# Performance work log

Hardware: AMD Instinct MI355X
Metric: run time of the kernel (lower is better)

## Reference

```python
import jax, jax.numpy as jnp
import numpy as np

K, R, D = 200000, 64, 1024
N_IDS = 16384
BITS = 4
GROUP = 32


def group_quantize(w, bits, group_size):
    """Group-wise symmetric fake-quant along the last dim (STE in bwd)."""
    last = w.shape[-1]
    g = min(group_size, last)
    n_groups = last // g
    wg = w.reshape(w.shape[:-1] + (n_groups, g))
    amax = jnp.clip(jnp.max(jnp.abs(wg), axis=-1, keepdims=True), 1e-8, None)
    q_max = (1 << (bits - 1)) - 1  # matches torch `1 << bits - 1` precedence
    scale = amax / q_max
    q = jnp.clip(jnp.round(wg / scale), -q_max, q_max) * scale
    # straight-through estimator: forward = q, backward = identity w.r.t. wg
    wq = wg + jax.lax.stop_gradient(q - wg)
    return wq.reshape(w.shape)


def setup_inputs() -> dict:
    key = jax.random.key(0)
    k1, k2, k3 = jax.random.split(key, 3)
    U = jax.random.normal(k1, (K, R), dtype=jnp.float32)
    B = jax.random.normal(k2, (R, D), dtype=jnp.float32)
    local_ids = jax.random.randint(k3, (N_IDS,), 0, K, dtype=jnp.int64 if jax.config.read('jax_enable_x64') else jnp.int32)
    return {"U": U, "B": B, "local_ids": local_ids}


def reference(U, B, local_ids):
    # row(): quantize ALL of U, gather selected rows, matmul with quantized B
    Uq = group_quantize(U, BITS, min(GROUP, R))   # [K, r]
    Bq = group_quantize(B, BITS, min(GROUP, D))   # [r, d]
    return Uq[local_ids] @ Bq                      # [N, d]
```

## Files before the change

### kernel.cpp

```cpp
#include <hip/hip_runtime.h>


#define R_DIM 64
#define D_DIM 1024
#define N_IDS 16384

#define BM 64
#define BN 128
#define LDS_STRIDE 72
#define OT_STRIDE 132

#define NB_QB 256
#define NB_QU 4096

typedef __attribute__((ext_vector_type(8))) __bf16 bf16x8;
typedef __attribute__((ext_vector_type(4))) float f32x4;

__device__ inline unsigned short f32_to_bf16_rne(float f) {
  union { float f; unsigned int u; } c; c.f = f;
  unsigned int u = c.u;
  u += 0x7fffu + ((u >> 16) & 1u);
  return (unsigned short)(u >> 16);
}

__device__ inline float bf16_bits_to_f32(unsigned short h) {
  union { unsigned int u; float f; } c; c.u = ((unsigned int)h) << 16;
  return c.f;
}

__device__ inline void quant_split(float w, float a, unsigned short* hi, unsigned short* lo) {
  double amax  = fmax((double)a, 1e-8);
  double scale = amax / 7.0;
  double t     = (double)w / scale;
  double q     = fmin(fmax(rint(t), -7.0), 7.0) * scale;
  float qf = (float)q;
  unsigned short h = f32_to_bf16_rne(qf);
  *hi = h;
  *lo = f32_to_bf16_rne(qf - bf16_bits_to_f32(h));
}

__device__ inline float group_amax32(float w) {
  float a = fabsf(w);
  a = fmaxf(a, __shfl_xor(a, 1));
  a = fmaxf(a, __shfl_xor(a, 2));
  a = fmaxf(a, __shfl_xor(a, 4));
  a = fmaxf(a, __shfl_xor(a, 8));
  a = fmaxf(a, __shfl_xor(a, 16));
  return a;
}

__global__ __launch_bounds__(256) void quant_fused_kernel(
    const float* __restrict__ U, const float* __restrict__ B,
    const int* __restrict__ ids,
    unsigned short* __restrict__ BqT_hi, unsigned short* __restrict__ BqT_lo,
    unsigned short* __restrict__ Uq_hi,  unsigned short* __restrict__ Uq_lo) {
  const int bid = blockIdx.x;
  if (bid < NB_QB) {
    int e = bid * 256 + threadIdx.x;
    int r = e >> 10;
    int c = e & 1023;
    float w = B[e];
    unsigned short hi, lo;
    quant_split(w, group_amax32(w), &hi, &lo);
    BqT_hi[c * R_DIM + r] = hi;
    BqT_lo[c * R_DIM + r] = lo;
  } else {
    int e = (bid - NB_QB) * 256 + threadIdx.x;
    int n = e >> 6;
    int r = e & 63;
    float w = __builtin_nontemporal_load(&U[(size_t)ids[n] * R_DIM + r]);
    unsigned short hi, lo;
    quant_split(w, group_amax32(w), &hi, &lo);
    Uq_hi[e] = hi;
    Uq_lo[e] = lo;
  }
}

__global__ __launch_bounds__(256) void gemm_kernel(
    const unsigned short* __restrict__ Uq_hi, const unsigned short* __restrict__ Uq_lo,
    const unsigned short* __restrict__ BqT_hi, const unsigned short* __restrict__ BqT_lo,
    float* __restrict__ out) {
  __shared__ char smem[2 * BN * LDS_STRIDE * 2];
  unsigned short* bt_hi = (unsigned short*)smem;
  unsigned short* bt_lo = bt_hi + BN * LDS_STRIDE;
  float* ot = (float*)smem;

  const int tid  = threadIdx.x;
  const int lane = tid & 63;
  const int wave = tid >> 6;
  const int bx   = blockIdx.x;
  const int nb   = bx & 7;
  const int mb   = bx >> 3;
  const int n0   = nb * BN;

  {
    const uint4* src_hi = (const uint4*)(BqT_hi + (size_t)n0 * R_DIM);
    const uint4* src_lo = (const uint4*)(BqT_lo + (size_t)n0 * R_DIM);
    #pragma unroll
    for (int it = 0; it < 4; ++it) {
      int c = tid + it * 256;
      int row = c >> 3, off = c & 7;
      *(uint4*)&bt_hi[row * LDS_STRIDE + off * 8] = src_hi[c];
      *(uint4*)&bt_lo[row * LDS_STRIDE + off * 8] = src_lo[c];
    }
  }

  const int m0    = mb * BM + wave * 16;
  const int arow  = m0 + (lane & 15);
  const int koff  = (lane >> 4) * 8;
  const int nlane = lane & 15;

  bf16x8 afrag_hi[2], afrag_lo[2];
  #pragma unroll
  for (int s = 0; s < 2; ++s) {
    afrag_hi[s] = *(const bf16x8*)&Uq_hi[(size_t)arow * R_DIM + s * 32 + koff];
    afrag_lo[s] = *(const bf16x8*)&Uq_lo[(size_t)arow * R_DIM + s * 32 + koff];
  }

  __syncthreads();

  f32x4 acc[8];
  #pragma unroll
  for (int nf = 0; nf < 8; ++nf) acc[nf] = (f32x4){0.f, 0.f, 0.f, 0.f};

  #pragma unroll
  for (int nf = 0; nf < 8; ++nf) {
    #pragma unroll
    for (int s = 0; s < 2; ++s) {
      const int boff = (nf * 16 + nlane) * LDS_STRIDE + s * 32 + koff;
      union { uint4 u; bf16x8 b; } bh, bl;
      bh.u = *(const uint4*)&bt_hi[boff];
      bl.u = *(const uint4*)&bt_lo[boff];
      acc[nf] = __builtin_amdgcn_mfma_f32_16x16x32_bf16(afrag_hi[s], bh.b, acc[nf], 0, 0, 0);
      acc[nf] = __builtin_amdgcn_mfma_f32_16x16x32_bf16(afrag_hi[s], bl.b, acc[nf], 0, 0, 0);
      acc[nf] = __builtin_amdgcn_mfma_f32_16x16x32_bf16(afrag_lo[s], bh.b, acc[nf], 0, 0, 0);
    }
  }

  __syncthreads();

  float* w = ot + wave * 16 * OT_STRIDE;
  {
    const int r0 = (lane >> 4) << 2;
    #pragma unroll
    for (int nf = 0; nf < 8; ++nf) {
      #pragma unroll
      for (int i = 0; i < 4; ++i) {
        w[(r0 + i) * OT_STRIDE + nlane + nf * 16] = acc[nf][i];
      }
    }
  }
  #pragma unroll
  for (int j = 0; j < 8; ++j) {
    const int row = j * 2 + (lane >> 5);
    f32x4 v = *(const f32x4*)&w[row * OT_STRIDE + (lane & 31) * 4];
    __builtin_nontemporal_store(v,
        (f32x4*)&out[(size_t)(m0 + row) * D_DIM + n0 + (lane & 31) * 4]);
  }
}

extern "C" void kernel_launch(void* const* d_in, const int* in_sizes, int n_in,
                              void* d_out, int out_size, void* d_ws, size_t ws_size,
                              hipStream_t stream) {
  const float* U   = (const float*)d_in[0];
  const float* B   = (const float*)d_in[1];
  const int*   ids = (const int*)d_in[2];
  float* out = (float*)d_out;

  unsigned short* BqT_hi = (unsigned short*)d_ws;
  unsigned short* BqT_lo = BqT_hi + R_DIM * D_DIM;
  unsigned short* Uq_hi  = BqT_lo + R_DIM * D_DIM;
  unsigned short* Uq_lo  = Uq_hi + (size_t)N_IDS * R_DIM;

  quant_fused_kernel<<<NB_QB + NB_QU, 256, 0, stream>>>(U, B, ids, BqT_hi, BqT_lo, Uq_hi, Uq_lo);
  gemm_kernel<<<(N_IDS / BM) * (D_DIM / BN), 256, 0, stream>>>(Uq_hi, Uq_lo, BqT_hi, BqT_lo, out);
}
```

Measured before the change: 30.68 us.

## Fuse U gather and quantization into GEMM A-fragment load

Moves the gather of U rows by ids and their group quantization into the GEMM kernel, where each lane loads 8 floats and reduces the group max across lanes with two shuffles. The separate quant kernel now handles only B, so the intermediate Uq hi/lo buffers are no longer written to or read back from global memory. In exchange, each U row is gathered and quantized 8 times (once per N-block), which adds redundant fp64 quant math and repeated gather traffic to the GEMM.

```diff
diff --git a/kernel.cpp b/kernel.cpp
--- a/kernel.cpp
+++ b/kernel.cpp
@@ -9,9 +9,6 @@
 #define BN 128
 #define LDS_STRIDE 72
 #define OT_STRIDE 132
-
-#define NB_QB 256
-#define NB_QU 4096
 
 typedef __attribute__((ext_vector_type(8))) __bf16 bf16x8;
 typedef __attribute__((ext_vector_type(4))) float f32x4;
@@ -39,45 +36,27 @@
   *lo = f32_to_bf16_rne(qf - bf16_bits_to_f32(h));
 }
 
-__device__ inline float group_amax32(float w) {
+__global__ __launch_bounds__(256) void quantB_kernel(
+    const float* __restrict__ B,
+    unsigned short* __restrict__ BqT_hi, unsigned short* __restrict__ BqT_lo) {
+  int e = blockIdx.x * 256 + threadIdx.x;
+  int r = e >> 10;
+  int c = e & 1023;
+  float w = B[e];
   float a = fabsf(w);
   a = fmaxf(a, __shfl_xor(a, 1));
   a = fmaxf(a, __shfl_xor(a, 2));
   a = fmaxf(a, __shfl_xor(a, 4));
   a = fmaxf(a, __shfl_xor(a, 8));
   a = fmaxf(a, __shfl_xor(a, 16));
-  return a;
-}
-
-__global__ __launch_bounds__(256) void quant_fused_kernel(
-    const float* __restrict__ U, const float* __restrict__ B,
-    const int* __restrict__ ids,
-    unsigned short* __restrict__ BqT_hi, unsigned short* __restrict__ BqT_lo,
-    unsigned short* __restrict__ Uq_hi,  unsigned short* __restrict__ Uq_lo) {
-  const int bid = blockIdx.x;
-  if (bid < NB_QB) {
-    int e = bid * 256 + threadIdx.x;
-    int r = e >> 10;
-    int c = e & 1023;
-    float w = B[e];
-    unsigned short hi, lo;
-    quant_split(w, group_amax32(w), &hi, &lo);
-    BqT_hi[c * R_DIM + r] = hi;
-    BqT_lo[c * R_DIM + r] = lo;
-  } else {
-    int e = (bid - NB_QB) * 256 + threadIdx.x;
-    int n = e >> 6;
-    int r = e & 63;
-    float w = __builtin_nontemporal_load(&U[(size_t)ids[n] * R_DIM + r]);
-    unsigned short hi, lo;
-    quant_split(w, group_amax32(w), &hi, &lo);
-    Uq_hi[e] = hi;
-    Uq_lo[e] = lo;
-  }
+  unsigned short hi, lo;
+  quant_split(w, a, &hi, &lo);
+  BqT_hi[c * R_DIM + r] = hi;
+  BqT_lo[c * R_DIM + r] = lo;
 }
 
 __global__ __launch_bounds__(256) void gemm_kernel(
-    const unsigned short* __restrict__ Uq_hi, const unsigned short* __restrict__ Uq_lo,
+    const float* __restrict__ U, const int* __restrict__ ids,
     const unsigned short* __restrict__ BqT_hi, const unsigned short* __restrict__ BqT_lo,
     float* __restrict__ out) {
   __shared__ char smem[2 * BN * LDS_STRIDE * 2];
@@ -106,15 +85,32 @@
   }
 
   const int m0    = mb * BM + wave * 16;
-  const int arow  = m0 + (lane & 15);
+  const int rowid = ids[m0 + (lane & 15)];
   const int koff  = (lane >> 4) * 8;
   const int nlane = lane & 15;
+  const float* urow = U + (size_t)rowid * R_DIM;
 
   bf16x8 afrag_hi[2], afrag_lo[2];
   #pragma unroll
   for (int s = 0; s < 2; ++s) {
-    afrag_hi[s] = *(const bf16x8*)&Uq_hi[(size_t)arow * R_DIM + s * 32 + koff];
-    afrag_lo[s] = *(const bf16x8*)&Uq_lo[(size_t)arow * R_DIM + s * 32 + koff];
+    float4 w0 = *(const float4*)(urow + s * 32 + koff);
+    float4 w1 = *(const float4*)(urow + s * 32 + koff + 4);
+    float wv[8] = {w0.x, w0.y, w0.z, w0.w, w1.x, w1.y, w1.z, w1.w};
+    float a = 0.0f;
+    #pragma unroll
+    for (int j = 0; j < 8; ++j) a = fmaxf(a, fabsf(wv[j]));
+    a = fmaxf(a, __shfl_xor(a, 16));
+    a = fmaxf(a, __shfl_xor(a, 32));
+    union { unsigned short s8[8]; bf16x8 b; } uh, ul;
+    #pragma unroll
+    for (int j = 0; j < 8; ++j) {
+      unsigned short hi, lo;
+      quant_split(wv[j], a, &hi, &lo);
+      uh.s8[j] = hi;
+      ul.s8[j] = lo;
+    }
+    afrag_hi[s] = uh.b;
+    afrag_lo[s] = ul.b;
   }
 
   __syncthreads();
@@ -169,9 +165,7 @@
 
   unsigned short* BqT_hi = (unsigned short*)d_ws;
   unsigned short* BqT_lo = BqT_hi + R_DIM * D_DIM;
-  unsigned short* Uq_hi  = BqT_lo + R_DIM * D_DIM;
-  unsigned short* Uq_lo  = Uq_hi + (size_t)N_IDS * R_DIM;
 
-  quant_fused_kernel<<<NB_QB + NB_QU, 256, 0, stream>>>(U, B, ids, BqT_hi, BqT_lo, Uq_hi, Uq_lo);
-  gemm_kernel<<<(N_IDS / BM) * (D_DIM / BN), 256, 0, stream>>>(Uq_hi, Uq_lo, BqT_hi, BqT_lo, out);
+  quantB_kernel<<<(R_DIM * D_DIM) / 256, 256, 0, stream>>>(B, BqT_hi, BqT_lo);
+  gemm_kernel<<<(N_IDS / BM) * (D_DIM / BN), 256, 0, stream>>>(U, ids, BqT_hi, BqT_lo, out);
 }
```

New measurement: 27.29 us. 11.0% less time.
